# Kernel tuning notes

Measured on AMD Instinct MI355X. Metric: run time of the kernel, lower is better.

The kernel has to match this reference:

```python
import jax, jax.numpy as jnp
import numpy as np

R = 1.3       # coordinate scale divisor
CL = 32       # Tucker rank / channels per plane
NL = 256      # plane resolution
NPTS = 262144 # number of query points


def _grid_sample_bilinear(plane, grid):
    """torch.nn.functional.grid_sample, mode='bilinear', padding_mode='zeros',
    align_corners=True, for a single (C,H,W) plane and (N,2) grid in [-1,1].
    grid[:,0] indexes W (x), grid[:,1] indexes H (y). Returns (N,C)."""
    C, H, W = plane.shape
    x = (grid[:, 0] + 1.0) * 0.5 * (W - 1)
    y = (grid[:, 1] + 1.0) * 0.5 * (H - 1)
    x0 = jnp.floor(x)
    y0 = jnp.floor(y)
    wx1 = x - x0
    wy1 = y - y0
    wx0 = 1.0 - wx1
    wy0 = 1.0 - wy1
    x0i = x0.astype(jnp.int32)
    y0i = y0.astype(jnp.int32)
    x1i = x0i + 1
    y1i = y0i + 1
    flat = plane.reshape(C, H * W)

    def tap(ix, iy, w):
        valid = (ix >= 0) & (ix < W) & (iy >= 0) & (iy < H)
        idx = jnp.clip(iy, 0, H - 1) * W + jnp.clip(ix, 0, W - 1)
        vals = flat[:, idx]                      # (C, N)
        return jnp.where(valid[None, :], vals, 0.0) * w[None, :]

    out = (tap(x0i, y0i, wx0 * wy0) + tap(x1i, y0i, wx1 * wy0)
           + tap(x0i, y1i, wx0 * wy1) + tap(x1i, y1i, wx1 * wy1))
    return out.T  # (N, C)


def setup_inputs() -> dict:
    key = jax.random.key(0)
    k0, k1, k2, k3, k4 = jax.random.split(key, 5)
    coordinates = jax.random.normal(k0, (1, NPTS, 3), dtype=jnp.float32)
    plane_xy = jax.random.normal(k1, (CL, NL, NL), dtype=jnp.float32) * 0.001
    plane_yz = jax.random.normal(k2, (CL, NL, NL), dtype=jnp.float32) * 0.001
    plane_xz = jax.random.normal(k3, (CL, NL, NL), dtype=jnp.float32) * 0.001
    G = jax.random.uniform(k4, (CL, CL, CL), dtype=jnp.float32) * 0.4 + 0.1
    return {"coordinates": coordinates, "plane_xy": plane_xy,
            "plane_yz": plane_yz, "plane_xz": plane_xz, "G": G}


def reference(coordinates, plane_xy, plane_yz, plane_xz, G):
    coords = coordinates[0] / R               # (N, 3), batch assumed 1 (squeeze(0))
    xy = _grid_sample_bilinear(plane_xy, coords[:, 0:2])   # (N, Cl)
    yz = _grid_sample_bilinear(plane_yz, coords[:, 1:3])   # (N, Cl)
    xz = _grid_sample_bilinear(plane_xz, coords[:, 0:3:2]) # (N, Cl)
    # Tucker core contraction: out[n] = sum_xyz G[x,y,z] xy[n,x] yz[n,y] xz[n,z]
    return jnp.einsum('xyz,nx,ny,nz->n', G, xy, yz, xz)
```

## Files before the change

### kernel.cpp

```cpp
#include <hip/hip_runtime.h>
#include <stdint.h>

typedef unsigned int uint;
typedef unsigned short ushort;

#define NPTS  262144
#define PLANE_T_ELEMS (65536 * 32)
#define PLANE_T_BYTES ((size_t)PLANE_T_ELEMS * 2)
#define WS_PLANES_BYTES ((size_t)3 * PLANE_T_ELEMS * 2)
#define WS_GRB_OFF  WS_PLANES_BYTES
#define WS_NEEDED   (WS_PLANES_BYTES + (size_t)32768 * 2)

typedef __attribute__((ext_vector_type(8))) short bf16x8;
typedef __attribute__((ext_vector_type(4))) float f32x4;
typedef __attribute__((ext_vector_type(2))) float f32x2;

__device__ __forceinline__ ushort f2bf(float f) {
  union { float f; uint u; } v; v.f = f;
  uint r = v.u + 0x7fffu + ((v.u >> 16) & 1u);
  return (ushort)(r >> 16);
}
__device__ __forceinline__ float bf_lo(uint u) {
  union { uint u; float f; } v; v.u = u << 16; return v.f;
}
__device__ __forceinline__ float bf_hi(uint u) {
  union { uint u; float f; } v; v.u = u & 0xffff0000u; return v.f;
}
__device__ __forceinline__ float b2f(ushort u) {
  union { uint u; float f; } v; v.u = (uint)u << 16; return v.f;
}


__global__ __launch_bounds__(256) void transpose_planes_k(
    const float* __restrict__ pxy, const float* __restrict__ pyz,
    const float* __restrict__ pxz, ushort* __restrict__ out) {
  int plane = blockIdx.x >> 8;
  int h = blockIdx.x & 255;
  const float* src = (plane == 0) ? pxy : (plane == 1) ? pyz : pxz;
  int w = threadIdx.x;
  int p = (h << 8) + w;
  uint vals[16];
#pragma unroll
  for (int c = 0; c < 32; c += 2) {
    float f0 = src[(size_t)c * 65536 + p];
    float f1 = src[(size_t)(c + 1) * 65536 + p];
    vals[c >> 1] = (uint)f2bf(f0) | ((uint)f2bf(f1) << 16);
  }
  uint4* d4 = (uint4*)(out + (size_t)plane * PLANE_T_ELEMS + (size_t)p * 32);
#pragma unroll
  for (int i = 0; i < 4; ++i)
    d4[i] = make_uint4(vals[4 * i], vals[4 * i + 1], vals[4 * i + 2], vals[4 * i + 3]);
}

__global__ __launch_bounds__(256) void prep_grb_k(const float* __restrict__ g,
                                                  ushort* __restrict__ grb) {
  int e = blockIdx.x * 256 + threadIdx.x;
  int j = e & 7;
  int l = (e >> 3) & 63;
  int xh = (e >> 9) & 1;
  int y = e >> 10;
  int x = xh * 16 + (l & 15);
  int z = ((l >> 4) << 3) + j;
  grb[e] = f2bf(g[x * 1024 + y * 32 + z]);
}

template <bool BIG, class F>
__device__ __forceinline__ void sample_plane(const ushort* __restrict__ bt,
                                             const float* __restrict__ bf,
                                             float gw, float gh, F store) {
  float fx = (gw + 1.0f) * 0.5f * 255.0f;
  float fy = (gh + 1.0f) * 0.5f * 255.0f;
  float fx0 = floorf(fx), fy0 = floorf(fy);
  float wx1 = fx - fx0, wy1 = fy - fy0;
  float wx0 = 1.0f - wx1, wy0 = 1.0f - wy1;
  int ix0 = (int)fx0, iy0 = (int)fy0;
  int ix1 = ix0 + 1, iy1 = iy0 + 1;
  bool vx0 = (ix0 >= 0) & (ix0 < 256);
  bool vx1 = (ix1 >= 0) & (ix1 < 256);
  bool vy0 = (iy0 >= 0) & (iy0 < 256);
  bool vy1 = (iy1 >= 0) & (iy1 < 256);
  float w00 = (vx0 & vy0) ? wx0 * wy0 : 0.0f;
  float w10 = (vx1 & vy0) ? wx1 * wy0 : 0.0f;
  float w01 = (vx0 & vy1) ? wx0 * wy1 : 0.0f;
  float w11 = (vx1 & vy1) ? wx1 * wy1 : 0.0f;
  int cx0 = min(max(ix0, 0), 255), cx1 = min(max(ix1, 0), 255);
  int cy0 = min(max(iy0, 0), 255), cy1 = min(max(iy1, 0), 255);
  if (BIG) {
    uint o00 = (uint)(((cy0 << 8) + cx0) << 6);
    uint o10 = (uint)(((cy0 << 8) + cx1) << 6);
    uint o01 = (uint)(((cy1 << 8) + cx0) << 6);
    uint o11 = (uint)(((cy1 << 8) + cx1) << 6);
    const char* base = (const char*)bt;
#pragma unroll
    for (int cc = 0; cc < 32; cc += 8) {
      uint4 a = *(const uint4*)(base + o00 + cc * 2);
      uint4 b = *(const uint4*)(base + o10 + cc * 2);
      uint4 c = *(const uint4*)(base + o01 + cc * 2);
      uint4 d = *(const uint4*)(base + o11 + cc * 2);
      const uint* pa = (const uint*)&a; const uint* pb = (const uint*)&b;
      const uint* pc = (const uint*)&c; const uint* pd = (const uint*)&d;
#pragma unroll
      for (int j = 0; j < 4; ++j) {
        float v0 = w00 * bf_lo(pa[j]) + w10 * bf_lo(pb[j]) +
                   w01 * bf_lo(pc[j]) + w11 * bf_lo(pd[j]);
        float v1 = w00 * bf_hi(pa[j]) + w10 * bf_hi(pb[j]) +
                   w01 * bf_hi(pc[j]) + w11 * bf_hi(pd[j]);
        store(cc + 2 * j, v0);
        store(cc + 2 * j + 1, v1);
      }
    }
  } else {
    int o00 = (cy0 << 8) + cx0, o10 = (cy0 << 8) + cx1;
    int o01 = (cy1 << 8) + cx0, o11 = (cy1 << 8) + cx1;
#pragma unroll
    for (int c = 0; c < 32; ++c) {
      const float* base = bf + (size_t)c * 65536;
      float v = w00 * base[o00] + w10 * base[o10] + w01 * base[o01] + w11 * base[o11];
      store(c, v);
    }
  }
}

__global__ __launch_bounds__(256, 4) void tucker_mfma_k(
    const float* __restrict__ coords,
    const ushort* __restrict__ planes_t,
    const ushort* __restrict__ grb,
    float* __restrict__ out) {
  __shared__ ushort xy_s[128][36];
  __shared__ ushort xz_s[128][40];
  __shared__ ushort yz_s[128][36];
  __shared__ float part_s[4][128];

  int tid = threadIdx.x;
  int l = tid & 63;
  int wv = tid >> 6;
  int s = l & 15;
  int kb = l >> 4;

  int q = tid & 127;
  int p = blockIdx.x * 128 + q;
  float c0c = coords[3 * p + 0] * (1.0f / 1.3f);
  float c1c = coords[3 * p + 1] * (1.0f / 1.3f);
  float c2c = coords[3 * p + 2] * (1.0f / 1.3f);

  if (tid < 128) {
    uint buf[16];
    auto pack = [&](int c, float v) {
      ushort h = f2bf(v);
      if (c & 1) buf[c >> 1] |= ((uint)h << 16);
      else buf[c >> 1] = (uint)h;
    };
    sample_plane<true>(planes_t, nullptr, c0c, c1c, pack);
    uint2* r2 = (uint2*)xy_s[q];
#pragma unroll
    for (int i = 0; i < 8; ++i) r2[i] = make_uint2(buf[2 * i], buf[2 * i + 1]);
    sample_plane<true>(planes_t + (size_t)PLANE_T_ELEMS, nullptr, c1c, c2c, pack);
    r2 = (uint2*)yz_s[q];
#pragma unroll
    for (int i = 0; i < 8; ++i) r2[i] = make_uint2(buf[2 * i], buf[2 * i + 1]);
  } else {
    uint buf[16];
    auto pack = [&](int c, float v) {
      ushort h = f2bf(v);
      if (c & 1) buf[c >> 1] |= ((uint)h << 16);
      else buf[c >> 1] = (uint)h;
    };
    sample_plane<true>(planes_t + (size_t)2 * PLANE_T_ELEMS, nullptr, c0c, c2c, pack);
    uint4* r4 = (uint4*)xz_s[q];
#pragma unroll
    for (int i = 0; i < 4; ++i)
      r4[i] = make_uint4(buf[4 * i], buf[4 * i + 1], buf[4 * i + 2], buf[4 * i + 3]);
  }

  const char* gb = (const char*)grb;
  uint lbase = (uint)l * 16;
  bf16x8 greg[8][2];
#pragma unroll
  for (int yl = 0; yl < 8; ++yl) {
#pragma unroll
    for (int h = 0; h < 2; ++h)
      greg[yl][h] =
          *(const bf16x8*)(gb + (uint)((wv * 8 + yl) * 2048 + h * 1024) + lbase);
  }
#pragma unroll
  for (int yl = 0; yl < 8; ++yl) {
    asm volatile("" : "+v"(greg[yl][0]));
    asm volatile("" : "+v"(greg[yl][1]));
  }
  __syncthreads();

  f32x4 zero = {0.f, 0.f, 0.f, 0.f};
#pragma unroll 2
  for (int t = 0; t < 8; ++t) {
    int pt = t * 16 + s;
    union BF { uint4 u; bf16x8 v; } bfrag;
    bfrag.u = *(const uint4*)(&xz_s[pt][0] + kb * 8);
    const ushort* yr = yz_s[pt];
    uint yp[4];
    yp[0] = *(const uint*)(yr + wv * 8 + 0);
    yp[1] = *(const uint*)(yr + wv * 8 + 2);
    yp[2] = *(const uint*)(yr + wv * 8 + 4);
    yp[3] = *(const uint*)(yr + wv * 8 + 6);

    f32x2 acc0 = {0.f, 0.f}, acc1 = {0.f, 0.f};
    f32x2 acc2 = {0.f, 0.f}, acc3 = {0.f, 0.f};
#pragma unroll
    for (int qq = 0; qq < 4; ++qq) {
#pragma unroll
      for (int par = 0; par < 2; ++par) {
        float yv = par ? bf_hi(yp[qq]) : bf_lo(yp[qq]);
        union D { f32x4 v; f32x2 h[2]; } d0, d1;
        d0.v = __builtin_amdgcn_mfma_f32_16x16x32_bf16(greg[2 * qq + par][0],
                                                       bfrag.v, zero, 0, 0, 0);
        d1.v = __builtin_amdgcn_mfma_f32_16x16x32_bf16(greg[2 * qq + par][1],
                                                       bfrag.v, zero, 0, 0, 0);
        f32x2 yvv = {yv, yv};
        acc0 += d0.h[0] * yvv;
        acc1 += d0.h[1] * yvv;
        acc2 += d1.h[0] * yvv;
        acc3 += d1.h[1] * yvv;
      }
    }

    const uint* xyr = (const uint*)xy_s[pt];
    uint q0 = xyr[kb * 2], q1 = xyr[kb * 2 + 1];
    uint q2 = xyr[8 + kb * 2], q3 = xyr[8 + kb * 2 + 1];
    float v = acc0[0] * bf_lo(q0) + acc0[1] * bf_hi(q0)
            + acc1[0] * bf_lo(q1) + acc1[1] * bf_hi(q1)
            + acc2[0] * bf_lo(q2) + acc2[1] * bf_hi(q2)
            + acc3[0] * bf_lo(q3) + acc3[1] * bf_hi(q3);
    v += __shfl_xor(v, 16, 64);
    v += __shfl_xor(v, 32, 64);
    if (l < 16) part_s[wv][pt] = v;
  }
  __syncthreads();

  if (tid < 128)
    out[blockIdx.x * 128 + tid] =
        part_s[0][tid] + part_s[1][tid] + part_s[2][tid] + part_s[3][tid];
}

__global__ __launch_bounds__(256) void tucker_small_k(
    const float* __restrict__ coords,
    const float* __restrict__ pxy, const float* __restrict__ pyz,
    const float* __restrict__ pxz, const float* __restrict__ g,
    float* __restrict__ out) {
  __shared__ float s_yz[256 * 33];
  int tid = threadIdx.x;
  int p = blockIdx.x * 256 + tid;
  float c0 = coords[3 * p + 0] / 1.3f;
  float c1 = coords[3 * p + 1] / 1.3f;
  float c2 = coords[3 * p + 2] / 1.3f;
  float xy[32], xz[32];
  float* yzrow = &s_yz[tid * 33];
  sample_plane<false>(nullptr, pxy, c0, c1, [&](int c, float v) { xy[c] = v; });
  sample_plane<false>(nullptr, pyz, c1, c2, [&](int c, float v) { yzrow[c] = v; });
  sample_plane<false>(nullptr, pxz, c0, c2, [&](int c, float v) { xz[c] = v; });
  float acc = 0.0f;
  for (int y = 0; y < 32; ++y) {
    float yzv = yzrow[y];
    float accy = 0.0f;
#pragma unroll
    for (int z = 0; z < 32; ++z) {
      float t0 = 0.f, t1 = 0.f, t2 = 0.f, t3 = 0.f;
#pragma unroll
      for (int x = 0; x < 32; x += 4) {
        t0 = fmaf(g[(x + 0) * 1024 + y * 32 + z], xy[x + 0], t0);
        t1 = fmaf(g[(x + 1) * 1024 + y * 32 + z], xy[x + 1], t1);
        t2 = fmaf(g[(x + 2) * 1024 + y * 32 + z], xy[x + 2], t2);
        t3 = fmaf(g[(x + 3) * 1024 + y * 32 + z], xy[x + 3], t3);
      }
      accy = fmaf((t0 + t1) + (t2 + t3), xz[z], accy);
    }
    acc = fmaf(accy, yzv, acc);
  }
  out[p] = acc;
}

extern "C" void kernel_launch(void* const* d_in, const int* in_sizes, int n_in,
                              void* d_out, int out_size, void* d_ws, size_t ws_size,
                              hipStream_t stream) {
  const float* coords = (const float*)d_in[0];
  const float* pxy = (const float*)d_in[1];
  const float* pyz = (const float*)d_in[2];
  const float* pxz = (const float*)d_in[3];
  const float* g   = (const float*)d_in[4];
  float* out = (float*)d_out;

  if (ws_size >= WS_NEEDED) {
    ushort* planes_t = (ushort*)d_ws;
    ushort* grb = (ushort*)((char*)d_ws + WS_GRB_OFF);
    hipLaunchKernelGGL(transpose_planes_k, dim3(768), dim3(256), 0, stream,
                       pxy, pyz, pxz, planes_t);
    hipLaunchKernelGGL(prep_grb_k, dim3(128), dim3(256), 0, stream, g, grb);
    hipLaunchKernelGGL(tucker_mfma_k, dim3(NPTS / 128), dim3(256), 0, stream,
                       coords, planes_t, grb, out);
  } else {
    hipLaunchKernelGGL(tucker_small_k, dim3(NPTS / 256), dim3(256), 0, stream,
                       coords, pxy, pyz, pxz, g, out);
  }
}
```

Before: 60.21 us.

## Bucket-sort query points by spatial cell to improve plane gather locality

Adds a counting-sort preprocessing pipeline of histogram, scan and scatter kernels. It groups points into 16x16x16 spatial cells and builds a permutation that the main MFMA kernel uses to read coordinates and write outputs. The intent is to make the bilinear gathers from the transposed bf16 planes hit cache more often, since neighbouring points share texels. In exchange it adds four extra kernel launches, atomics over 262k points, a single-block serial scan, and scattered output writes. The zero_hist kernel clears 4096 bins, which is the full key range.

```diff
diff --git a/kernel.cpp b/kernel.cpp
--- a/kernel.cpp
+++ b/kernel.cpp
@@ -9,7 +9,10 @@
 #define PLANE_T_BYTES ((size_t)PLANE_T_ELEMS * 2)
 #define WS_PLANES_BYTES ((size_t)3 * PLANE_T_ELEMS * 2)
 #define WS_GRB_OFF  WS_PLANES_BYTES
-#define WS_NEEDED   (WS_PLANES_BYTES + (size_t)32768 * 2)
+#define WS_HIST_OFF (WS_GRB_OFF + 65536)
+#define WS_PERM_OFF (WS_HIST_OFF + 16384)
+#define WS_NEEDED       (WS_GRB_OFF + 65536)
+#define WS_SORT_NEEDED  (WS_PERM_OFF + (size_t)NPTS * 4)
 
 typedef __attribute__((ext_vector_type(8))) short bf16x8;
 typedef __attribute__((ext_vector_type(4))) float f32x4;
@@ -62,6 +65,56 @@
   int x = xh * 16 + (l & 15);
   int z = ((l >> 4) << 3) + j;
   grb[e] = f2bf(g[x * 1024 + y * 32 + z]);
+}
+
+__device__ __forceinline__ int cellkey(float c0, float c1, float c2) {
+  float fx = (c0 * (1.0f / 1.3f) + 1.0f) * 0.5f * 255.0f;
+  float fy = (c1 * (1.0f / 1.3f) + 1.0f) * 0.5f * 255.0f;
+  float fz = (c2 * (1.0f / 1.3f) + 1.0f) * 0.5f * 255.0f;
+  int ix = min(max((int)fx, 0), 255);
+  int iy = min(max((int)fy, 0), 255);
+  int iz = min(max((int)fz, 0), 255);
+  return ((ix >> 4) << 8) | ((iy >> 4) << 4) | (iz >> 4);
+}
+
+__global__ __launch_bounds__(256) void zero_hist_k(int* __restrict__ hist) {
+  hist[blockIdx.x * 256 + threadIdx.x] = 0;
+}
+
+__global__ __launch_bounds__(256) void hist_k(const float* __restrict__ coords,
+                                              int* __restrict__ hist) {
+  int p = blockIdx.x * 256 + threadIdx.x;
+  atomicAdd(&hist[cellkey(coords[3 * p], coords[3 * p + 1], coords[3 * p + 2])], 1);
+}
+
+__global__ __launch_bounds__(256) void scan_k(int* __restrict__ hist) {
+  __shared__ int sums[256];
+  int t = threadIdx.x;
+  int base = t * 16;
+  int v[16];
+  int sum = 0;
+#pragma unroll
+  for (int i = 0; i < 16; ++i) { v[i] = hist[base + i]; sum += v[i]; }
+  sums[t] = sum;
+  __syncthreads();
+  if (t == 0) {
+    int acc = 0;
+#pragma unroll 4
+    for (int i = 0; i < 256; ++i) { int x = sums[i]; sums[i] = acc; acc += x; }
+  }
+  __syncthreads();
+  int acc = sums[t];
+#pragma unroll
+  for (int i = 0; i < 16; ++i) { int x = v[i]; hist[base + i] = acc; acc += x; }
+}
+
+__global__ __launch_bounds__(256) void scatter_k(const float* __restrict__ coords,
+                                                 int* __restrict__ off,
+                                                 int* __restrict__ perm) {
+  int p = blockIdx.x * 256 + threadIdx.x;
+  int pos = atomicAdd(
+      &off[cellkey(coords[3 * p], coords[3 * p + 1], coords[3 * p + 2])], 1);
+  perm[pos] = p;
 }
 
 template <bool BIG, class F>
@@ -125,6 +178,7 @@
     const float* __restrict__ coords,
     const ushort* __restrict__ planes_t,
     const ushort* __restrict__ grb,
+    const int* __restrict__ perm,
     float* __restrict__ out) {
   __shared__ ushort xy_s[128][36];
   __shared__ ushort xz_s[128][40];
@@ -138,7 +192,8 @@
   int kb = l >> 4;
 
   int q = tid & 127;
-  int p = blockIdx.x * 128 + q;
+  int idx = blockIdx.x * 128 + q;
+  int p = perm ? perm[idx] : idx;
   float c0c = coords[3 * p + 0] * (1.0f / 1.3f);
   float c1c = coords[3 * p + 1] * (1.0f / 1.3f);
   float c2c = coords[3 * p + 2] * (1.0f / 1.3f);
@@ -235,9 +290,11 @@
   }
   __syncthreads();
 
-  if (tid < 128)
-    out[blockIdx.x * 128 + tid] =
-        part_s[0][tid] + part_s[1][tid] + part_s[2][tid] + part_s[3][tid];
+  if (tid < 128) {
+    int oidx = blockIdx.x * 128 + tid;
+    int po = perm ? perm[oidx] : oidx;
+    out[po] = part_s[0][tid] + part_s[1][tid] + part_s[2][tid] + part_s[3][tid];
+  }
 }
 
 __global__ __launch_bounds__(256) void tucker_small_k(
@@ -293,8 +350,19 @@
     hipLaunchKernelGGL(transpose_planes_k, dim3(768), dim3(256), 0, stream,
                        pxy, pyz, pxz, planes_t);
     hipLaunchKernelGGL(prep_grb_k, dim3(128), dim3(256), 0, stream, g, grb);
+    int* perm = nullptr;
+    if (ws_size >= WS_SORT_NEEDED) {
+      int* hist = (int*)((char*)d_ws + WS_HIST_OFF);
+      perm = (int*)((char*)d_ws + WS_PERM_OFF);
+      hipLaunchKernelGGL(zero_hist_k, dim3(16), dim3(256), 0, stream, hist);
+      hipLaunchKernelGGL(hist_k, dim3(NPTS / 256), dim3(256), 0, stream, coords,
+                         hist);
+      hipLaunchKernelGGL(scan_k, dim3(1), dim3(256), 0, stream, hist);
+      hipLaunchKernelGGL(scatter_k, dim3(NPTS / 256), dim3(256), 0, stream, coords,
+                         hist, perm);
+    }
     hipLaunchKernelGGL(tucker_mfma_k, dim3(NPTS / 128), dim3(256), 0, stream,
-                       coords, planes_t, grb, out);
+                       coords, planes_t, grb, perm, out);
   } else {
     hipLaunchKernelGGL(tucker_small_k, dim3(NPTS / 256), dim3(256), 0, stream,
                        coords, pxy, pyz, pxz, g, out);
```

Measured after the change: 141.0 us. 2.34x slower.
